# Kernel tuning notes

Hardware: AMD Instinct MI355X
Metric: run time of the kernel (lower is better)

The kernel has to match this reference:

```python
import jax, jax.numpy as jnp
import numpy as np

DIM = 192
HEADS = 6
WIN = (2, 6, 12)          # (pl, lat, lon)
TOW = 64                  # type_of_windows = (8//2)*(96//6)
N_TOK = WIN[0] * WIN[1] * WIN[2]            # 144
TABLE_ROWS = WIN[0]**2 * WIN[1]**2 * (2 * WIN[2] - 1)  # 3312


def calc_position_bias_indices(size):
    pl, la, lo = size
    plq = np.arange(pl); plk = -np.arange(pl) * pl
    laq = np.arange(la); lak = -np.arange(la) * la
    lon = np.arange(lo)
    gq = np.stack(np.meshgrid(plq, laq, lon, indexing='ij'))  # [3,pl,la,lo]
    gk = np.stack(np.meshgrid(plk, lak, lon, indexing='ij'))
    fq = gq.reshape(3, -1)
    fk = gk.reshape(3, -1)
    d = fq[:, :, None] - fk[:, None, :]          # [3,N,N]
    d = np.transpose(d, (1, 2, 0)).copy()
    d[:, :, 2] += lo - 1
    d[:, :, 1] *= 2 * lo - 1
    d[:, :, 0] *= (2 * lo - 1) * la * la
    return d.sum(-1)                              # [N,N]


def setup_inputs() -> dict:
    key = jax.random.key(0)
    ks = jax.random.split(key, 7)
    B_, nW, N, C = 15, TOW, N_TOK, DIM
    x = jax.random.normal(ks[0], (B_, nW, N, C), jnp.float32)
    mask = jax.random.normal(ks[1], (15, nW, N, N), jnp.float32)  # nLon=15
    qkv_w = jax.random.normal(ks[2], (3 * C, C), jnp.float32) * 0.02
    qkv_b = jnp.zeros((3 * C,), jnp.float32)
    table = jax.random.normal(ks[3], (TABLE_ROWS, TOW, HEADS), jnp.float32) * 0.02
    proj_w = jax.random.normal(ks[4], (C, C), jnp.float32) * 0.02
    proj_b = jnp.zeros((C,), jnp.float32)
    pos_index = jnp.asarray(calc_position_bias_indices(WIN), jnp.int32)  # [N,N]
    return {"x": x, "mask": mask, "qkv_w": qkv_w, "qkv_b": qkv_b,
            "table": table, "proj_w": proj_w, "proj_b": proj_b,
            "pos_index": pos_index}


def reference(x, mask, qkv_w, qkv_b, table, proj_w, proj_b, pos_index):
    B_, nW, N, C = x.shape
    h = HEADS
    hd = C // h
    scale = hd ** -0.5
    # qkv projection -> (3, B_, h, nW, N, hd)
    qkv = (jnp.einsum('bwnc,dc->bwnd', x, qkv_w) + qkv_b)
    qkv = qkv.reshape(B_, nW, N, 3, h, hd).transpose(3, 0, 4, 1, 2, 5)
    q, k, v = qkv[0] * scale, qkv[1], qkv[2]
    attn = jnp.einsum('bhwqd,bhwkd->bhwqk', q, k)      # [B_,h,nW,N,N]
    # gather earth position bias: [N,N,tow,h] -> [h,tow,N,N]
    bias = table[pos_index.reshape(-1)].reshape(N, N, nW, h)
    bias = bias.transpose(3, 2, 0, 1)
    attn = attn + bias[None]
    nLon = mask.shape[0]
    attn = attn.reshape(B_ // nLon, nLon, h, nW, N, N) + mask[None, :, None]
    attn = attn.reshape(B_, h, nW, N, N)
    attn = jax.nn.softmax(attn, axis=-1)
    out = jnp.einsum('bhwqk,bhwkd->bhwqd', attn, v)
    out = out.transpose(0, 2, 3, 1, 4).reshape(B_, nW, N, C)
    return jnp.einsum('bwnc,dc->bwnd', out, proj_w) + proj_b
```

## Files before the change

kernel.cpp:

```cpp
#include <hip/hip_runtime.h>

#define HEADS 6
#define N_TOK 144
#define DIM   192
#define NW    64
#define NB    15
#define NBW   (NB * NW)
#define CHUNK 480

typedef __attribute__((ext_vector_type(8))) short bf16x8;
typedef __attribute__((ext_vector_type(4))) float f32x4;

#define MFMA(a, b, c) __builtin_amdgcn_mfma_f32_16x16x32_bf16(a, b, c, 0, 0, 0)

static __device__ __forceinline__ short f2bf(float f) {
    union { float f; unsigned u; } v; v.f = f;
    unsigned r = v.u + 0x7FFFu + ((v.u >> 16) & 1u);
    return (short)(r >> 16);
}
static __device__ __forceinline__ float bf2f(short s) {
    union { unsigned u; float f; } v;
    v.u = ((unsigned)(unsigned short)s) << 16;
    return v.f;
}
static __device__ __forceinline__ unsigned pk2(float a, float b) {
    return (unsigned)(unsigned short)f2bf(a) |
           ((unsigned)(unsigned short)f2bf(b) << 16);
}

__global__ __launch_bounds__(256)
void bias_k(const float* __restrict__ table, const int* __restrict__ pos_index,
            short* __restrict__ bias_bf) {
    const int t = blockIdx.x;
    for (int e = threadIdx.x; e < N_TOK * N_TOK; e += 256) {
        int idx = pos_index[e];
        bias_bf[(long)t * (N_TOK * N_TOK) + e] = f2bf(table[(long)idx * 384 + t]);
    }
}

__global__ __launch_bounds__(256)
void cvt_k(const float* __restrict__ w, short* __restrict__ o, int n) {
    int i = blockIdx.x * 256 + threadIdx.x;
    if (i < n) o[i] = f2bf(w[i]);
}

__global__ __launch_bounds__(192)
void qkvs192_k(const float* __restrict__ x, const short* __restrict__ qkvw_bf,
               const float* __restrict__ qkv_b, short* __restrict__ qk_ws,
               short* __restrict__ vT_ws, int bw0) {
    __shared__ short xl[192 * 56];

    const int p = blockIdx.x;
    const int l = (p & 7) * 540 + (p >> 3);
    const int mg  = l % 3;
    const int sel = (l / 3) % 3;
    const int bwL = l / 9;
    const int bwG = bw0 + bwL;
    const int tid = threadIdx.x;

    {
        const float* xg = x + ((long)bwG * N_TOK + mg * 48) * DIM;
        for (int u = tid * 4; u < 48 * DIM; u += 192 * 4) {
            float4 f = *(const float4*)&xg[u];
            short4 s = { f2bf(f.x), f2bf(f.y), f2bf(f.z), f2bf(f.w) };
            int r = u / DIM, c = u - r * DIM;
            *(short4*)&xl[r * 200 + c] = s;
        }
    }
    __syncthreads();

    const int wid = tid >> 6, lane = tid & 63, lq = lane & 15, lg = lane >> 4;
    const int ng = wid;

    f32x4 acc[3][4] = {};
    for (int ks = 0; ks < 6; ++ks) {
        const int k0 = ks * 32 + 8 * lg;
        bf16x8 av[3], bv[4];
        #pragma unroll
        for (int mt = 0; mt < 3; ++mt)
            av[mt] = *(const bf16x8*)&xl[(mt * 16 + lq) * 200 + k0];
        #pragma unroll
        for (int nt = 0; nt < 4; ++nt)
            bv[nt] = *(const bf16x8*)&qkvw_bf[
                ((long)sel * 192 + ng * 64 + nt * 16 + lq) * 192 + k0];
        #pragma unroll
        for (int mt = 0; mt < 3; ++mt)
            #pragma unroll
            for (int nt = 0; nt < 4; ++nt)
                acc[mt][nt] = MFMA(av[mt], bv[nt], acc[mt][nt]);
    }
    __syncthreads();

    const float scale = 0.17677669529663687f;

    if (sel < 2) {
        #pragma unroll
        for (int nt = 0; nt < 4; ++nt) {
            const int cd = ng * 64 + nt * 16 + lq;
            const float bb = qkv_b[sel * 192 + cd];
            #pragma unroll
            for (int mt = 0; mt < 3; ++mt)
                #pragma unroll
                for (int i = 0; i < 4; ++i) {
                    int row = mt * 16 + 4 * lg + i;
                    float v = acc[mt][nt][i] + bb;
                    if (sel == 0) v *= scale;
                    xl[row * 200 + cd] = f2bf(v);
                }
        }
        __syncthreads();
        short* ob = qk_ws + (long)bwL * 6 * 2 * 4608 + (long)sel * 4608
                  + mg * 48 * 32;
        #pragma unroll
        for (int j = 0; j < 6; ++j) {
            int u = (j * 192 + tid) * 8;
            int h = u / 1536, rem = u - h * 1536;
            int row = rem >> 5, e = rem & 31;
            *(bf16x8*)&ob[(long)h * 2 * 4608 + row * 32 + e] =
                *(const bf16x8*)&xl[row * 200 + h * 32 + e];
        }
    } else {
        #pragma unroll
        for (int nt = 0; nt < 4; ++nt) {
            const int cd = ng * 64 + nt * 16 + lq;
            const float bb = qkv_b[2 * 192 + cd];
            #pragma unroll
            for (int mt = 0; mt < 3; ++mt)
                #pragma unroll
                for (int i = 0; i < 4; ++i) {
                    int row = mt * 16 + 4 * lg + i;
                    xl[cd * 56 + row] = f2bf(acc[mt][nt][i] + bb);
                }
        }
        __syncthreads();
        short* ob = vT_ws + (long)bwL * 6 * 4608 + mg * 48;
        #pragma unroll
        for (int j = 0; j < 6; ++j) {
            int u = (j * 192 + tid) * 8;
            int he = u / 48, row0 = u - he * 48;
            *(bf16x8*)&ob[(long)he * 144 + row0] =
                *(const bf16x8*)&xl[he * 56 + row0];
        }
    }
}

__global__ __launch_bounds__(192, 6)
void attn3w_k(const short* __restrict__ qk_ws, const short* __restrict__ vT_ws,
              const short* __restrict__ bias_bf, const float* __restrict__ mask,
              short* __restrict__ tmp, int bw0) {
    __shared__ short pws[3 * 16 * 168];

    const int p = blockIdx.x;
    const int l = (p & 7) * 1080 + (p >> 3);
    const int third = l % 3;
    const int h     = (l / 3) % HEADS;
    const int bwL   = l / 18;
    const int bwG   = bw0 + bwL;
    const int lane = threadIdx.x & 63, lq = lane & 15, lg = lane >> 4;
    const int wid = threadIdx.x >> 6;
    const int mt9 = third * 3 + wid;
    const int q = mt9 * 16 + lq;
    const int w = bwG & 63;

    const short* qb = qk_ws + (long)(bwL * 6 + h) * 2 * 4608;
    const short* kb = qb + 4608;

    const f32x4 zf = {};
    bf16x8 bq = *(const bf16x8*)&qb[q * 32 + 8 * lg];
    f32x4 lgt[9];
    #pragma unroll
    for (int nt = 0; nt < 9; ++nt) {
        bf16x8 ak = *(const bf16x8*)&kb[(nt * 16 + lq) * 32 + 8 * lg];
        lgt[nt] = MFMA(ak, bq, zf);
    }

    const short* bp = bias_bf + (long)(w * 6 + h) * (N_TOK * N_TOK)
                    + q * N_TOK + 4 * lg;
    const float* mp = mask + (long)bwG * (N_TOK * N_TOK) + q * N_TOK + 4 * lg;
    #pragma unroll
    for (int nt = 0; nt < 9; ++nt) {
        short4 bs = *(const short4*)&bp[nt * 16];
        float4 mf = *(const float4*)&mp[nt * 16];
        lgt[nt][0] += bf2f(bs.x) + mf.x;
        lgt[nt][1] += bf2f(bs.y) + mf.y;
        lgt[nt][2] += bf2f(bs.z) + mf.z;
        lgt[nt][3] += bf2f(bs.w) + mf.w;
    }

    float m = lgt[0][0];
    #pragma unroll
    for (int nt = 0; nt < 9; ++nt)
        #pragma unroll
        for (int i = 0; i < 4; ++i) m = fmaxf(m, lgt[nt][i]);
    m = fmaxf(m, __shfl_xor(m, 16));
    m = fmaxf(m, __shfl_xor(m, 32));
    float s = 0.f;
    #pragma unroll
    for (int nt = 0; nt < 9; ++nt)
        #pragma unroll
        for (int i = 0; i < 4; ++i) {
            float pe = __expf(lgt[nt][i] - m);
            lgt[nt][i] = pe;
            s += pe;
        }
    s += __shfl_xor(s, 16);
    s += __shfl_xor(s, 32);
    const float inv = 1.f / s;

    short* pw = pws + wid * 16 * 168;
    #pragma unroll
    for (int nt = 0; nt < 9; ++nt) {
        *(unsigned*)&pw[lq * 168 + nt * 16 + 4 * lg]     = pk2(lgt[nt][0], lgt[nt][1]);
        *(unsigned*)&pw[lq * 168 + nt * 16 + 4 * lg + 2] = pk2(lgt[nt][2], lgt[nt][3]);
    }

    const short* vsrc = vT_ws + (long)(bwL * 6 + h) * 4608;
    f32x4 o[2] = {};
    const bf16x8 zb = {};
    #pragma unroll
    for (int kt = 0; kt < 5; ++kt) {
        bf16x8 bpf = *(const bf16x8*)&pw[lq * 168 + kt * 32 + 8 * lg];
        #pragma unroll
        for (int et = 0; et < 2; ++et) {
            bf16x8 av = *(const bf16x8*)&vsrc[(et * 16 + lq) * N_TOK + kt * 32 + 8 * lg];
            bf16x8 aa = av, bb = bpf;
            if (kt == 4 && lg >= 2) { aa = zb; bb = zb; }
            o[et] = MFMA(aa, bb, o[et]);
        }
    }

    short* tb = tmp + ((long)bwL * N_TOK + q) * DIM + h * 32;
    #pragma unroll
    for (int et = 0; et < 2; ++et) {
        short4 sx = { f2bf(o[et][0] * inv), f2bf(o[et][1] * inv),
                      f2bf(o[et][2] * inv), f2bf(o[et][3] * inv) };
        *(short4*)&tb[et * 16 + 4 * lg] = sx;
    }
}

__global__ __launch_bounds__(192)
void proj_k(const short* __restrict__ tmp, const short* __restrict__ pwt,
            const float* __restrict__ proj_b, float* __restrict__ out, int bw0) {
    const int bid = blockIdx.x;
    const int mthird = bid % 3;
    const int bwL = bid / 3;
    const int bwG = bw0 + bwL;
    const int tid = threadIdx.x;
    const int wid = tid >> 6, lane = tid & 63, lq = lane & 15, lg = lane >> 4;
    const int m0 = (mthird * 3 + wid) * 16;
    const short* tb = tmp + (long)bwL * N_TOK * DIM;

    f32x4 acc[12] = {};
    for (int ks = 0; ks < 6; ++ks) {
        const int k0 = ks * 32 + 8 * lg;
        bf16x8 a = *(const bf16x8*)&tb[(m0 + lq) * DIM + k0];
        #pragma unroll
        for (int nt = 0; nt < 12; ++nt) {
            bf16x8 b = *(const bf16x8*)&pwt[(nt * 16 + lq) * DIM + k0];
            acc[nt] = MFMA(a, b, acc[nt]);
        }
    }
    float* ob = out + (long)bwG * N_TOK * DIM;
    #pragma unroll
    for (int nt = 0; nt < 12; ++nt) {
        float pb = proj_b[nt * 16 + lq];
        #pragma unroll
        for (int i = 0; i < 4; ++i)
            ob[(m0 + 4 * lg + i) * DIM + nt * 16 + lq] = acc[nt][i] + pb;
    }
}

extern "C" void kernel_launch(void* const* d_in, const int* in_sizes, int n_in,
                              void* d_out, int out_size, void* d_ws, size_t ws_size,
                              hipStream_t stream) {
    const float* x        = (const float*)d_in[0];
    const float* mask     = (const float*)d_in[1];
    const float* qkv_w    = (const float*)d_in[2];
    const float* qkv_b    = (const float*)d_in[3];
    const float* table    = (const float*)d_in[4];
    const float* proj_w   = (const float*)d_in[5];
    const float* proj_b   = (const float*)d_in[6];
    const int*   pos_index= (const int*)d_in[7];
    float* out = (float*)d_out;

    short* bias_bf  = (short*)d_ws;
    short* projw_bf = bias_bf + (size_t)384 * N_TOK * N_TOK;
    short* qkvw_bf  = projw_bf + 36864;
    short* tmp_ws   = qkvw_bf + 110592;
    short* qk_ws    = tmp_ws + (size_t)CHUNK * N_TOK * DIM;
    short* vT_ws    = qk_ws + (size_t)CHUNK * 6 * 2 * 4608;

    bias_k<<<384, 256, 0, stream>>>(table, pos_index, bias_bf);
    cvt_k<<<144, 256, 0, stream>>>(proj_w, projw_bf, DIM * DIM);
    cvt_k<<<432, 256, 0, stream>>>(qkv_w, qkvw_bf, 3 * DIM * DIM);

    for (int c = 0; c < 2; ++c) {
        const int bw0 = c * CHUNK;
        qkvs192_k<<<CHUNK * 9, 192, 0, stream>>>(x, qkvw_bf, qkv_b,
                                                 qk_ws, vT_ws, bw0);
        attn3w_k<<<CHUNK * 18, 192, 0, stream>>>(qk_ws, vT_ws, bias_bf, mask,
                                                 tmp_ws, bw0);
        proj_k<<<CHUNK * 3, 192, 0, stream>>>(tmp_ws, projw_bf, proj_b, out, bw0);
    }
}
```

Before: 464.5 us.

## Prefetch V fragments early in attention kernel, use packed bf16 conversions

Loads the V fragments into registers before the bias/mask/softmax phase so their global latency overlaps the softmax work, instead of loading them inside the PV MFMA loop. Adds s_setprio around the MFMA sections, replaces the manual bf16 rounding with HIP packed conversion intrinsics, and zero-pads the tail of the P tile in shared memory. The minimum-blocks-per-CU hint for the attention kernel drops from 6 to 4 to leave room for the extra registers, which may reduce occupancy.

New measurement: 459.4 us. Within noise of the previous version (-1.1%).

```diff
diff --git a/kernel.cpp b/kernel.cpp
--- a/kernel.cpp
+++ b/kernel.cpp
@@ -1,4 +1,5 @@
 #include <hip/hip_runtime.h>
+#include <hip/hip_bf16.h>
 
 #define HEADS 6
 #define N_TOK 144
@@ -14,9 +15,8 @@
 #define MFMA(a, b, c) __builtin_amdgcn_mfma_f32_16x16x32_bf16(a, b, c, 0, 0, 0)
 
 static __device__ __forceinline__ short f2bf(float f) {
-    union { float f; unsigned u; } v; v.f = f;
-    unsigned r = v.u + 0x7FFFu + ((v.u >> 16) & 1u);
-    return (short)(r >> 16);
+    __hip_bfloat16 h = __float2bfloat16(f);
+    return *reinterpret_cast<short*>(&h);
 }
 static __device__ __forceinline__ float bf2f(short s) {
     union { unsigned u; float f; } v;
@@ -24,8 +24,8 @@
     return v.f;
 }
 static __device__ __forceinline__ unsigned pk2(float a, float b) {
-    return (unsigned)(unsigned short)f2bf(a) |
-           ((unsigned)(unsigned short)f2bf(b) << 16);
+    __hip_bfloat162 h = __float22bfloat162_rn(make_float2(a, b));
+    return *reinterpret_cast<unsigned*>(&h);
 }
 
 __global__ __launch_bounds__(256)
@@ -62,9 +62,9 @@
         const float* xg = x + ((long)bwG * N_TOK + mg * 48) * DIM;
         for (int u = tid * 4; u < 48 * DIM; u += 192 * 4) {
             float4 f = *(const float4*)&xg[u];
-            short4 s = { f2bf(f.x), f2bf(f.y), f2bf(f.z), f2bf(f.w) };
+            uint2 s = make_uint2(pk2(f.x, f.y), pk2(f.z, f.w));
             int r = u / DIM, c = u - r * DIM;
-            *(short4*)&xl[r * 200 + c] = s;
+            *(uint2*)&xl[r * 200 + c] = s;
         }
     }
     __syncthreads();
@@ -144,7 +144,7 @@
     }
 }
 
-__global__ __launch_bounds__(192, 6)
+__global__ __launch_bounds__(192, 4)
 void attn3w_k(const short* __restrict__ qk_ws, const short* __restrict__ vT_ws,
               const short* __restrict__ bias_bf, const float* __restrict__ mask,
               short* __restrict__ tmp, int bw0) {
@@ -168,10 +168,32 @@
     const f32x4 zf = {};
     bf16x8 bq = *(const bf16x8*)&qb[q * 32 + 8 * lg];
     f32x4 lgt[9];
+    __builtin_amdgcn_s_setprio(1);
     #pragma unroll
     for (int nt = 0; nt < 9; ++nt) {
         bf16x8 ak = *(const bf16x8*)&kb[(nt * 16 + lq) * 32 + 8 * lg];
         lgt[nt] = MFMA(ak, bq, zf);
+    }
+    __builtin_amdgcn_s_setprio(0);
+
+    const short* vsrc = vT_ws + (long)(bwL * 6 + h) * 4608;
+    bf16x8 vfr[10];
+    #pragma unroll
+    for (int kt = 0; kt < 4; ++kt)
+        #pragma unroll
+        for (int et = 0; et < 2; ++et)
+            vfr[kt * 2 + et] =
+                *(const bf16x8*)&vsrc[(et * 16 + lq) * N_TOK + kt * 32 + 8 * lg];
+    {
+        const int lgc = (lg < 2) ? lg : 0;
+        #pragma unroll
+        for (int et = 0; et < 2; ++et)
+            vfr[8 + et] =
+                *(const bf16x8*)&vsrc[(et * 16 + lq) * N_TOK + 128 + 8 * lgc];
+        if (lg >= 2) {
+            const bf16x8 zb = {};
+            vfr[8] = zb; vfr[9] = zb;
+        }
     }
 
     const short* bp = bias_bf + (long)(w * 6 + h) * (N_TOK * N_TOK)
@@ -210,31 +232,29 @@
     short* pw = pws + wid * 16 * 168;
     #pragma unroll
     for (int nt = 0; nt < 9; ++nt) {
-        *(unsigned*)&pw[lq * 168 + nt * 16 + 4 * lg]     = pk2(lgt[nt][0], lgt[nt][1]);
-        *(unsigned*)&pw[lq * 168 + nt * 16 + 4 * lg + 2] = pk2(lgt[nt][2], lgt[nt][3]);
-    }
-
-    const short* vsrc = vT_ws + (long)(bwL * 6 + h) * 4608;
+        uint2 u2 = make_uint2(pk2(lgt[nt][0], lgt[nt][1]),
+                              pk2(lgt[nt][2], lgt[nt][3]));
+        *(uint2*)&pw[lq * 168 + nt * 16 + 4 * lg] = u2;
+    }
+    *(uint2*)&pw[lq * 168 + 144 + 4 * lg] = make_uint2(0u, 0u);
+
     f32x4 o[2] = {};
-    const bf16x8 zb = {};
+    __builtin_amdgcn_s_setprio(1);
     #pragma unroll
     for (int kt = 0; kt < 5; ++kt) {
         bf16x8 bpf = *(const bf16x8*)&pw[lq * 168 + kt * 32 + 8 * lg];
         #pragma unroll
-        for (int et = 0; et < 2; ++et) {
-            bf16x8 av = *(const bf16x8*)&vsrc[(et * 16 + lq) * N_TOK + kt * 32 + 8 * lg];
-            bf16x8 aa = av, bb = bpf;
-            if (kt == 4 && lg >= 2) { aa = zb; bb = zb; }
-            o[et] = MFMA(aa, bb, o[et]);
-        }
-    }
+        for (int et = 0; et < 2; ++et)
+            o[et] = MFMA(vfr[kt * 2 + et], bpf, o[et]);
+    }
+    __builtin_amdgcn_s_setprio(0);
 
     short* tb = tmp + ((long)bwL * N_TOK + q) * DIM + h * 32;
     #pragma unroll
     for (int et = 0; et < 2; ++et) {
-        short4 sx = { f2bf(o[et][0] * inv), f2bf(o[et][1] * inv),
-                      f2bf(o[et][2] * inv), f2bf(o[et][3] * inv) };
-        *(short4*)&tb[et * 16 + 4 * lg] = sx;
+        uint2 u2 = make_uint2(pk2(o[et][0] * inv, o[et][1] * inv),
+                              pk2(o[et][2] * inv, o[et][3] * inv));
+        *(uint2*)&tb[et * 16 + 4 * lg] = u2;
     }
 }
 
```
